# Kernel optimization log

Measured on AMD Instinct MI355X. Metric: run time of the kernel, lower is better.

Reference implementation:

```python
import jax, jax.numpy as jnp
import numpy as np

D_MODEL = 1024
NUM_HEADS = 16
D_K = D_MODEL // NUM_HEADS
B, N = 4, 2048


def setup_inputs() -> dict:
    key = jax.random.key(0)
    ks = jax.random.split(key, 5)
    scale = 1.0 / np.sqrt(D_MODEL)
    return {
        "x": jax.random.normal(ks[0], (B, N, D_MODEL), dtype=jnp.float32),
        "wq": jax.random.normal(ks[1], (D_MODEL, D_MODEL), dtype=jnp.float32) * scale,
        "wk": jax.random.normal(ks[2], (D_MODEL, D_MODEL), dtype=jnp.float32) * scale,
        "wv": jax.random.normal(ks[3], (D_MODEL, D_MODEL), dtype=jnp.float32) * scale,
        "wo": jax.random.normal(ks[4], (D_MODEL, D_MODEL), dtype=jnp.float32) * scale,
    }


def reference(x, wq, wk, wv, wo):
    b, n, d = x.shape
    # torch Linear(weight W) computes x @ W.T
    def proj(w):
        return (x @ w.T).reshape(b, n, NUM_HEADS, D_K).transpose(0, 2, 1, 3)  # [B,H,N,d_k]
    Q, K, V = proj(wq), proj(wk), proj(wv)
    scores = jnp.einsum("bhqd,bhkd->bhqk", Q, K) / jnp.sqrt(jnp.float32(D_K))
    causal = jnp.tril(jnp.ones((n, n), dtype=bool))
    scores = jnp.where(causal, scores, jnp.float32(-jnp.inf))
    attn = jax.nn.softmax(scores, axis=-1)
    vals = jnp.einsum("bhqk,bhkd->bhqd", attn, V)  # [B,H,N,d_k]
    vals = vals.transpose(0, 2, 1, 3).reshape(b, n, d)
    out = vals @ wo.T
    return (out, K, V)
```

## Files before the change

### kernel.cpp

```cpp
#include <hip/hip_runtime.h>
#include <hip/hip_bf16.h>

typedef __bf16 bf16_t;
typedef __bf16 bf16x8 __attribute__((ext_vector_type(8)));
typedef __bf16 bf16x4 __attribute__((ext_vector_type(4)));
typedef float f32x4 __attribute__((ext_vector_type(4)));
typedef float f32x16 __attribute__((ext_vector_type(16)));
typedef int i32x4 __attribute__((ext_vector_type(4)));

#define LDS_AS __attribute__((address_space(3)))
#define GLB_AS __attribute__((address_space(1)))

__device__ __forceinline__ void gload_lds16(const void* g, void* l) {
  __builtin_amdgcn_global_load_lds((const GLB_AS void*)g, (LDS_AS void*)l, 16, 0, 0);
}

static __device__ __forceinline__ f32x4 mfma16(bf16x8 a, bf16x8 b, f32x4 c) {
  return __builtin_amdgcn_mfma_f32_16x16x32_bf16(a, b, c, 0, 0, 0);
}
static __device__ __forceinline__ f32x16 mfma32(bf16x8 a, bf16x8 b, f32x16 c) {
  return __builtin_amdgcn_mfma_f32_32x32x16_bf16(a, b, c, 0, 0, 0);
}
__device__ __forceinline__ int cvtpk_bf16(float lo, float hi) {
  int r;
  asm("v_cvt_pk_bf16_f32 %0, %1, %2" : "=v"(r) : "v"(lo), "v"(hi));
  return r;
}
__device__ __forceinline__ bf16x8 mkfrag(int w0, int w1, int w2, int w3) {
  i32x4 v;
  v[0] = w0; v[1] = w1; v[2] = w2; v[3] = w3;
  return __builtin_bit_cast(bf16x8, v);
}

#define PIPE_TILE_END()                                        \
  asm volatile("s_waitcnt vmcnt(0)" ::: "memory");             \
  __builtin_amdgcn_s_barrier();                                \
  asm volatile("" ::: "memory");                               \
  __builtin_amdgcn_sched_barrier(0)

__device__ __forceinline__ void xcd_rc(int orig, int& rowI, int& colI) {
  int logical = ((orig & 7) << 6) | (orig >> 3);
  rowI = logical >> 3;
  colI = logical & 7;
}

#define QSCALE 0.18033688011112042f

__global__ __launch_bounds__(256) void cast_kernel(
    const float* __restrict__ x, const float* __restrict__ wq,
    const float* __restrict__ wk, const float* __restrict__ wv,
    const float* __restrict__ wo, bf16_t* __restrict__ xb,
    bf16_t* __restrict__ wqb, bf16_t* __restrict__ wkb,
    bf16_t* __restrict__ wvb, bf16_t* __restrict__ wob) {
  size_t i = ((size_t)blockIdx.x * 256 + threadIdx.x) * 4;
  const float* s;
  bf16_t* d;
  size_t off;
  if (i < 8388608) {
    s = x; d = xb; off = i;
  } else {
    size_t j = i - 8388608;
    int wi = (int)(j >> 20);
    off = j & 1048575;
    s = wi == 0 ? wq : wi == 1 ? wk : wi == 2 ? wv : wo;
    d = wi == 0 ? wqb : wi == 1 ? wkb : wi == 2 ? wvb : wob;
  }
  float4 v = *(const float4*)(s + off);
  bf16x4 o;
  o[0] = (bf16_t)v.x; o[1] = (bf16_t)v.y; o[2] = (bf16_t)v.z; o[3] = (bf16_t)v.w;
  *(bf16x4*)(d + off) = o;
}

__global__ __launch_bounds__(512) void gemm_qkv(
    const bf16_t* __restrict__ xb, const bf16_t* __restrict__ wqb,
    const bf16_t* __restrict__ wkb, const bf16_t* __restrict__ wvb,
    bf16_t* __restrict__ Qb, bf16_t* __restrict__ Kb, bf16_t* __restrict__ vTb,
    float* __restrict__ outK, float* __restrict__ outV) {
  __shared__ __align__(16) bf16_t lds[32768];
  const int tid = threadIdx.x;
  const int lane = tid & 63, w = tid >> 6;
  const int llo = lane & 15, lhi = lane >> 4;
  const int wm = w >> 2, wn = w & 3;
  int rowI, colI;
  xcd_rc(blockIdx.x, rowI, colI);
  const int rowBase = rowI * 128, colW = colI * 128;

  const int arow = tid >> 2, asrc = (tid & 3) ^ ((arow >> 1) & 3);
  const bf16_t* srcA = xb + (size_t)(rowBase + arow) * 1024 + asrc * 8;
  const bf16_t* srcB0 = wqb + (size_t)(colW + arow) * 1024 + asrc * 8;
  const bf16_t* srcB1 = wkb + (size_t)(colW + arow) * 1024 + asrc * 8;
  const bf16_t* srcB2 = wvb + (size_t)(colW + arow) * 1024 + asrc * 8;
  const int dstA = tid * 8;
  const int dstB0 = 4096 + tid * 8;
  const int dstB1 = 4096 + (512 + tid) * 8;
  const int dstB2 = 4096 + (1024 + tid) * 8;

  auto STAGE = [&](int kt, int b) {
    bf16_t* base = lds + b * 16384;
    gload_lds16(srcA + kt * 32, base + dstA);
    gload_lds16(srcB0 + kt * 32, base + dstB0);
    gload_lds16(srcB1 + kt * 32, base + dstB1);
    gload_lds16(srcB2 + kt * 32, base + dstB2);
  };

  f32x4 acc[4][6] = {};
  const int xr = (llo >> 1) & 3;
  STAGE(0, 0);
  PIPE_TILE_END();
  for (int kt = 0; kt < 32; ++kt) {
    if (kt + 1 < 32) STAGE(kt + 1, (kt + 1) & 1);
    __builtin_amdgcn_sched_barrier(0);
    const bf16_t* bufA = lds + (kt & 1) * 16384;
    const bf16_t* bufB = bufA + 4096;
    bf16x8 aF[4], bF[6];
#pragma unroll
    for (int mf = 0; mf < 4; ++mf)
      aF[mf] = *(const bf16x8*)&bufA[(wm * 64 + mf * 16 + llo) * 32 +
                                     ((lhi ^ xr) * 8)];
#pragma unroll
    for (int nf = 0; nf < 6; ++nf)
      bF[nf] = *(const bf16x8*)&bufB[(wn * 96 + nf * 16 + llo) * 32 +
                                     ((lhi ^ xr) * 8)];
    __builtin_amdgcn_s_setprio(1);
#pragma unroll
    for (int mf = 0; mf < 4; ++mf)
#pragma unroll
      for (int nf = 0; nf < 6; ++nf) acc[mf][nf] = mfma16(aF[mf], bF[nf], acc[mf][nf]);
    __builtin_amdgcn_s_setprio(0);
    PIPE_TILE_END();
  }

#pragma unroll
  for (int mf = 0; mf < 4; ++mf) {
    int m0 = rowBase + wm * 64 + mf * 16 + lhi * 4;
    int b = m0 >> 11, tok0 = m0 & 2047;
#pragma unroll
    for (int nf = 0; nf < 6; ++nf) {
      int n = wn * 96 + nf * 16 + llo;
      int mat = n >> 7;
      int nm = colW + (n & 127);
      int h = nm >> 6, dk = nm & 63;
      size_t hoff = ((size_t)(b * 16 + h) * 2048 + tok0) * 64 + dk;
      if (mat == 0) {
#pragma unroll
        for (int r = 0; r < 4; ++r)
          Qb[hoff + (size_t)r * 64] = (bf16_t)(acc[mf][nf][r] * QSCALE);
      } else if (mat == 1) {
#pragma unroll
        for (int r = 0; r < 4; ++r) {
          outK[hoff + (size_t)r * 64] = acc[mf][nf][r];
          Kb[hoff + (size_t)r * 64] = (bf16_t)acc[mf][nf][r];
        }
      } else {
#pragma unroll
        for (int r = 0; r < 4; ++r) outV[hoff + (size_t)r * 64] = acc[mf][nf][r];
        bf16x4 pk;
#pragma unroll
        for (int r = 0; r < 4; ++r) pk[r] = (bf16_t)acc[mf][nf][r];
        *(bf16x4*)&vTb[((size_t)(b * 16 + h) * 64 + dk) * 2048 + tok0] = pk;
      }
    }
  }
}

__global__ __launch_bounds__(256) void gemm_out(const bf16_t* __restrict__ valsb,
                                                const bf16_t* __restrict__ wob,
                                                float* __restrict__ out) {
  __shared__ __align__(16) bf16_t lds[16384];
  const int tid = threadIdx.x;
  const int lane = tid & 63, w = tid >> 6;
  const int llo = lane & 15, lhi = lane >> 4;
  const int wm = w >> 1, wn = w & 1;
  int rowI, colI;
  xcd_rc(blockIdx.x, rowI, colI);
  const int rowBase = rowI * 128, colW = colI * 128;

  int g0 = tid, g1 = 256 + tid;
  int r0 = g0 >> 2, r1 = g1 >> 2;
  int s0 = (g0 & 3) ^ ((r0 >> 1) & 3), s1 = (g1 & 3) ^ ((r1 >> 1) & 3);
  const bf16_t* srcA0 = valsb + (size_t)(rowBase + r0) * 1024 + s0 * 8;
  const bf16_t* srcA1 = valsb + (size_t)(rowBase + r1) * 1024 + s1 * 8;
  const bf16_t* srcB0 = wob + (size_t)(colW + r0) * 1024 + s0 * 8;
  const bf16_t* srcB1 = wob + (size_t)(colW + r1) * 1024 + s1 * 8;
  const int dA0 = g0 * 8, dA1 = g1 * 8;
  const int dB0 = 4096 + g0 * 8, dB1 = 4096 + g1 * 8;

  auto STAGE = [&](int kt, int b) {
    bf16_t* base = lds + b * 8192;
    gload_lds16(srcA0 + kt * 32, base + dA0);
    gload_lds16(srcA1 + kt * 32, base + dA1);
    gload_lds16(srcB0 + kt * 32, base + dB0);
    gload_lds16(srcB1 + kt * 32, base + dB1);
  };

  f32x4 acc[4][4] = {};
  const int xr = (llo >> 1) & 3;
  STAGE(0, 0);
  PIPE_TILE_END();
  for (int kt = 0; kt < 32; ++kt) {
    if (kt + 1 < 32) STAGE(kt + 1, (kt + 1) & 1);
    __builtin_amdgcn_sched_barrier(0);
    const bf16_t* bufA = lds + (kt & 1) * 8192;
    const bf16_t* bufB = bufA + 4096;
    bf16x8 aF[4], bF[4];
#pragma unroll
    for (int mf = 0; mf < 4; ++mf)
      aF[mf] = *(const bf16x8*)&bufA[(wm * 64 + mf * 16 + llo) * 32 +
                                     ((lhi ^ xr) * 8)];
#pragma unroll
    for (int nf = 0; nf < 4; ++nf)
      bF[nf] = *(const bf16x8*)&bufB[(wn * 64 + nf * 16 + llo) * 32 +
                                     ((lhi ^ xr) * 8)];
    __builtin_amdgcn_s_setprio(1);
#pragma unroll
    for (int mf = 0; mf < 4; ++mf)
#pragma unroll
      for (int nf = 0; nf < 4; ++nf) acc[mf][nf] = mfma16(aF[mf], bF[nf], acc[mf][nf]);
    __builtin_amdgcn_s_setprio(0);
    PIPE_TILE_END();
  }
#pragma unroll
  for (int mf = 0; mf < 4; ++mf) {
    int m0 = rowBase + wm * 64 + mf * 16 + lhi * 4;
#pragma unroll
    for (int nf = 0; nf < 4; ++nf) {
      int n = colW + wn * 64 + nf * 16 + llo;
#pragma unroll
      for (int r = 0; r < 4; ++r) out[(size_t)(m0 + r) * 1024 + n] = acc[mf][nf][r];
    }
  }
}

__global__ __launch_bounds__(256, 3) void attn_kernel(
    const bf16_t* __restrict__ Qb, const bf16_t* __restrict__ Kb,
    const bf16_t* __restrict__ vTb, bf16_t* __restrict__ valsb) {
  __shared__ bf16_t kS[2][64 * 64];
  __shared__ bf16_t vS[2][64 * 64];
  const int tid = threadIdx.x;
  const int w = tid >> 6, lane = tid & 63;
  const int ql = lane & 31, hi = lane >> 5, hi4 = hi * 4;
  const int head = blockIdx.x;
  const int qseg = 15 - blockIdx.y;
  const int qbase = qseg * 128;
  const int qw = qbase + w * 32;
  const int qrow = qw + ql;
  const int nkt = qseg * 2 + 2;
  const bf16_t* Qh = Qb + (size_t)head * 131072;
  const bf16_t* Kh = Kb + (size_t)head * 131072;
  const bf16_t* Vh = vTb + (size_t)head * 131072;

  bf16x8 qB[4];
#pragma unroll
  for (int kk = 0; kk < 4; ++kk)
    qB[kk] = *(const bf16x8*)&Qh[(size_t)qrow * 64 + kk * 16 + hi * 8];

  i32x4 ov;
  ov[0] = ov[1] = ov[2] = ov[3] = 0x3F803F80;
  const bf16x8 onesF = __builtin_bit_cast(bf16x8, ov);

  f32x16 oacc0 = {}, oacc1 = {};
  f32x16 lacc = {};

  const int c0 = tid, c1 = 256 + tid;
  const int r0 = c0 >> 3, r1 = c1 >> 3;
  const int s0 = (c0 & 7) ^ ((r0 ^ (r0 >> 3)) & 7);
  const int s1 = (c1 & 7) ^ ((r1 ^ (r1 >> 3)) & 7);

  auto STAGE = [&](int kt_, int bi) {
    const int kb_ = kt_ * 64;
    gload_lds16(Kh + (size_t)(kb_ + r0) * 64 + s0 * 8, &kS[bi][c0 * 8]);
    gload_lds16(Kh + (size_t)(kb_ + r1) * 64 + s1 * 8, &kS[bi][c1 * 8]);
    gload_lds16(Vh + (size_t)r0 * 2048 + kb_ + s0 * 8, &vS[bi][c0 * 8]);
    gload_lds16(Vh + (size_t)r1 * 2048 + kb_ + s1 * 8, &vS[bi][c1 * 8]);
  };

  const int swzA = (ql ^ (ql >> 3)) & 7;
  const int swzB = swzA ^ 4;

  STAGE(0, 0);
  __syncthreads();
  int cur = 0;
  for (int kt = 0; kt < nkt; ++kt) {
    const int kbase = kt * 64;
    if (kt + 1 < nkt) STAGE(kt + 1, cur ^ 1);
    if (kbase <= qw) {
      const bf16_t* kb = kS[cur];
      const bf16_t* vb = vS[cur];
      f32x16 st0 = {}, st1 = {};
      __builtin_amdgcn_s_setprio(1);
#pragma unroll
      for (int kk = 0; kk < 4; ++kk) {
        bf16x8 kf0 = *(const bf16x8*)&kb[ql * 64 + (((kk * 2 + hi) ^ swzA) * 8)];
        st0 = mfma32(kf0, qB[kk], st0);
      }
#pragma unroll
      for (int kk = 0; kk < 4; ++kk) {
        bf16x8 kf1 = *(const bf16x8*)&kb[(32 + ql) * 64 + (((kk * 2 + hi) ^ swzB) * 8)];
        st1 = mfma32(kf1, qB[kk], st1);
      }
      __builtin_amdgcn_s_setprio(0);
      if (kbase + 64 > qw) {
        const int lim = qrow - kbase;
#pragma unroll
        for (int rg = 0; rg < 16; ++rg) {
          const int kof = (rg & 3) + 8 * (rg >> 2) + hi4;
          if (kof > lim) st0[rg] = -__builtin_inff();
          if (kof + 32 > lim) st1[rg] = -__builtin_inff();
        }
      }
#pragma unroll
      for (int j = 0; j < 16; ++j) {
        st0[j] = __builtin_amdgcn_exp2f(st0[j]);
        st1[j] = __builtin_amdgcn_exp2f(st1[j]);
      }
      int a0 = cvtpk_bf16(st0[0], st0[1]), a1 = cvtpk_bf16(st0[2], st0[3]);
      int a2 = cvtpk_bf16(st0[4], st0[5]), a3 = cvtpk_bf16(st0[6], st0[7]);
      int a4 = cvtpk_bf16(st0[8], st0[9]), a5 = cvtpk_bf16(st0[10], st0[11]);
      int a6 = cvtpk_bf16(st0[12], st0[13]), a7 = cvtpk_bf16(st0[14], st0[15]);
      int b0 = cvtpk_bf16(st1[0], st1[1]), b1 = cvtpk_bf16(st1[2], st1[3]);
      int b2 = cvtpk_bf16(st1[4], st1[5]), b3 = cvtpk_bf16(st1[6], st1[7]);
      int b4 = cvtpk_bf16(st1[8], st1[9]), b5 = cvtpk_bf16(st1[10], st1[11]);
      int b6 = cvtpk_bf16(st1[12], st1[13]), b7 = cvtpk_bf16(st1[14], st1[15]);
      auto s02 = __builtin_amdgcn_permlane32_swap(a0, a2, false, false);
      auto s13 = __builtin_amdgcn_permlane32_swap(a1, a3, false, false);
      auto s46 = __builtin_amdgcn_permlane32_swap(a4, a6, false, false);
      auto s57 = __builtin_amdgcn_permlane32_swap(a5, a7, false, false);
      auto t02 = __builtin_amdgcn_permlane32_swap(b0, b2, false, false);
      auto t13 = __builtin_amdgcn_permlane32_swap(b1, b3, false, false);
      auto t46 = __builtin_amdgcn_permlane32_swap(b4, b6, false, false);
      auto t57 = __builtin_amdgcn_permlane32_swap(b5, b7, false, false);
      bf16x8 pB0 = mkfrag(s02[0], s13[0], s02[1], s13[1]);
      bf16x8 pB1 = mkfrag(s46[0], s57[0], s46[1], s57[1]);
      bf16x8 pB2 = mkfrag(t02[0], t13[0], t02[1], t13[1]);
      bf16x8 pB3 = mkfrag(t46[0], t57[0], t46[1], t57[1]);
      __builtin_amdgcn_s_setprio(1);
#pragma unroll
      for (int ks = 0; ks < 4; ++ks) {
        bf16x8 pb = ks == 0 ? pB0 : ks == 1 ? pB1 : ks == 2 ? pB2 : pB3;
        bf16x8 vf0 = *(const bf16x8*)&vb[ql * 64 + (((ks * 2 + hi) ^ swzA) * 8)];
        oacc0 = mfma32(vf0, pb, oacc0);
        bf16x8 vf1 = *(const bf16x8*)&vb[(32 + ql) * 64 + (((ks * 2 + hi) ^ swzB) * 8)];
        oacc1 = mfma32(vf1, pb, oacc1);
        lacc = mfma32(onesF, pb, lacc);
      }
      __builtin_amdgcn_s_setprio(0);
    }
    __syncthreads();
    cur ^= 1;
  }
  const float inv = 1.f / lacc[0];
  size_t base = ((size_t)(head >> 4) * 2048 + qrow) * 1024 + (head & 15) * 64 + hi4;
#pragma unroll
  for (int rg = 0; rg < 4; ++rg) {
    bf16x4 o0, o1;
#pragma unroll
    for (int j = 0; j < 4; ++j) {
      o0[j] = (bf16_t)(oacc0[rg * 4 + j] * inv);
      o1[j] = (bf16_t)(oacc1[rg * 4 + j] * inv);
    }
    *(bf16x4*)&valsb[base + rg * 8] = o0;
    *(bf16x4*)&valsb[base + 32 + rg * 8] = o1;
  }
}

extern "C" void kernel_launch(void* const* d_in, const int* in_sizes, int n_in,
                              void* d_out, int out_size, void* d_ws, size_t ws_size,
                              hipStream_t stream) {
  const float* x = (const float*)d_in[0];
  const float* wq = (const float*)d_in[1];
  const float* wk = (const float*)d_in[2];
  const float* wv = (const float*)d_in[3];
  const float* wo = (const float*)d_in[4];
  float* out = (float*)d_out;
  float* outK = out + 8388608;
  float* outV = out + 16777216;
  bf16_t* xb = (bf16_t*)d_ws;
  bf16_t* wqb = xb + 8388608;
  bf16_t* wkb = wqb + 1048576;
  bf16_t* wvb = wkb + 1048576;
  bf16_t* wob = wvb + 1048576;
  bf16_t* Qb = wob + 1048576;
  bf16_t* Kb = Qb + 8388608;
  bf16_t* vTb = Kb + 8388608;
  bf16_t* valsb = vTb + 8388608;
  cast_kernel<<<12288, 256, 0, stream>>>(x, wq, wk, wv, wo, xb, wqb, wkb, wvb, wob);
  gemm_qkv<<<512, 512, 0, stream>>>(xb, wqb, wkb, wvb, Qb, Kb, vTb, outK, outV);
  attn_kernel<<<dim3(64, 16), 256, 0, stream>>>(Qb, Kb, vTb, valsb);
  gemm_out<<<512, 256, 0, stream>>>(valsb, wob, out);
}
```

Measured before the change: 160.3 us.

## Split attention key range across two wave groups and reduce partials in LDS

The attention block grows from 256 to 512 threads, and two groups of four waves each process alternating 64-key tiles of a 128-key stage. At the end, the partial output accumulators and row sums are combined through LDS. The row sum is now computed from the exponentials with VALU adds plus a lane shuffle, replacing the extra ones-matrix MFMA per step. This aims to double the waves working on each query tile and drop one MFMA per k-step, at the cost of an LDS reduction, a final sync, and launch bounds that allow one block per CU.

```diff
diff --git a/kernel.cpp b/kernel.cpp
--- a/kernel.cpp
+++ b/kernel.cpp
@@ -166,7 +166,7 @@
 __global__ __launch_bounds__(256) void gemm_out(const bf16_t* __restrict__ valsb,
                                                 const bf16_t* __restrict__ wob,
                                                 float* __restrict__ out) {
-  __shared__ __align__(16) bf16_t lds[16384];
+  __shared__ __align__(16) bf16_t slds[16384];
   const int tid = threadIdx.x;
   const int lane = tid & 63, w = tid >> 6;
   const int llo = lane & 15, lhi = lane >> 4;
@@ -186,7 +186,7 @@
   const int dB0 = 4096 + g0 * 8, dB1 = 4096 + g1 * 8;
 
   auto STAGE = [&](int kt, int b) {
-    bf16_t* base = lds + b * 8192;
+    bf16_t* base = slds + b * 8192;
     gload_lds16(srcA0 + kt * 32, base + dA0);
     gload_lds16(srcA1 + kt * 32, base + dA1);
     gload_lds16(srcB0 + kt * 32, base + dB0);
@@ -200,7 +200,7 @@
   for (int kt = 0; kt < 32; ++kt) {
     if (kt + 1 < 32) STAGE(kt + 1, (kt + 1) & 1);
     __builtin_amdgcn_sched_barrier(0);
-    const bf16_t* bufA = lds + (kt & 1) * 8192;
+    const bf16_t* bufA = slds + (kt & 1) * 8192;
     const bf16_t* bufB = bufA + 4096;
     bf16x8 aF[4], bF[4];
 #pragma unroll
@@ -231,20 +231,21 @@
   }
 }
 
-__global__ __launch_bounds__(256, 3) void attn_kernel(
+__global__ __launch_bounds__(512, 1) void attn_kernel(
     const bf16_t* __restrict__ Qb, const bf16_t* __restrict__ Kb,
     const bf16_t* __restrict__ vTb, bf16_t* __restrict__ valsb) {
-  __shared__ bf16_t kS[2][64 * 64];
-  __shared__ bf16_t vS[2][64 * 64];
+  __shared__ bf16_t kS[2][2][4096];
+  __shared__ bf16_t vS[2][2][4096];
   const int tid = threadIdx.x;
   const int w = tid >> 6, lane = tid & 63;
+  const int g = w >> 2, wq = w & 3;
   const int ql = lane & 31, hi = lane >> 5, hi4 = hi * 4;
   const int head = blockIdx.x;
   const int qseg = 15 - blockIdx.y;
   const int qbase = qseg * 128;
-  const int qw = qbase + w * 32;
+  const int qw = qbase + wq * 32;
   const int qrow = qw + ql;
-  const int nkt = qseg * 2 + 2;
+  const int nsi = qseg + 1;
   const bf16_t* Qh = Qb + (size_t)head * 131072;
   const bf16_t* Kh = Kb + (size_t)head * 131072;
   const bf16_t* Vh = vTb + (size_t)head * 131072;
@@ -254,38 +255,33 @@
   for (int kk = 0; kk < 4; ++kk)
     qB[kk] = *(const bf16x8*)&Qh[(size_t)qrow * 64 + kk * 16 + hi * 8];
 
-  i32x4 ov;
-  ov[0] = ov[1] = ov[2] = ov[3] = 0x3F803F80;
-  const bf16x8 onesF = __builtin_bit_cast(bf16x8, ov);
-
   f32x16 oacc0 = {}, oacc1 = {};
-  f32x16 lacc = {};
-
-  const int c0 = tid, c1 = 256 + tid;
-  const int r0 = c0 >> 3, r1 = c1 >> 3;
-  const int s0 = (c0 & 7) ^ ((r0 ^ (r0 >> 3)) & 7);
-  const int s1 = (c1 & 7) ^ ((r1 ^ (r1 >> 3)) & 7);
-
-  auto STAGE = [&](int kt_, int bi) {
-    const int kb_ = kt_ * 64;
-    gload_lds16(Kh + (size_t)(kb_ + r0) * 64 + s0 * 8, &kS[bi][c0 * 8]);
-    gload_lds16(Kh + (size_t)(kb_ + r1) * 64 + s1 * 8, &kS[bi][c1 * 8]);
-    gload_lds16(Vh + (size_t)r0 * 2048 + kb_ + s0 * 8, &vS[bi][c0 * 8]);
-    gload_lds16(Vh + (size_t)r1 * 2048 + kb_ + s1 * 8, &vS[bi][c1 * 8]);
+  float lsum = 0.f;
+
+  const int sr = tid >> 3;
+  const int sc = (tid & 7) ^ ((sr ^ (sr >> 3)) & 7);
+
+  auto STAGE = [&](int si) {
+    const int p = si & 1;
+    const int ka = si * 128;
+    const int kb2 = ka + 64;
+    gload_lds16(Kh + (size_t)(ka + sr) * 64 + sc * 8, &kS[p][0][tid * 8]);
+    gload_lds16(Vh + (size_t)sr * 2048 + ka + sc * 8, &vS[p][0][tid * 8]);
+    gload_lds16(Kh + (size_t)(kb2 + sr) * 64 + sc * 8, &kS[p][1][tid * 8]);
+    gload_lds16(Vh + (size_t)sr * 2048 + kb2 + sc * 8, &vS[p][1][tid * 8]);
   };
 
   const int swzA = (ql ^ (ql >> 3)) & 7;
   const int swzB = swzA ^ 4;
 
-  STAGE(0, 0);
+  STAGE(0);
   __syncthreads();
-  int cur = 0;
-  for (int kt = 0; kt < nkt; ++kt) {
-    const int kbase = kt * 64;
-    if (kt + 1 < nkt) STAGE(kt + 1, cur ^ 1);
+  for (int si = 0; si < nsi; ++si) {
+    if (si + 1 < nsi) STAGE(si + 1);
+    const int kbase = si * 128 + g * 64;
     if (kbase <= qw) {
-      const bf16_t* kb = kS[cur];
-      const bf16_t* vb = vS[cur];
+      const bf16_t* kb = kS[si & 1][g];
+      const bf16_t* vb = vS[si & 1][g];
       f32x16 st0 = {}, st1 = {};
       __builtin_amdgcn_s_setprio(1);
 #pragma unroll
@@ -308,11 +304,21 @@
           if (kof + 32 > lim) st1[rg] = -__builtin_inff();
         }
       }
-#pragma unroll
-      for (int j = 0; j < 16; ++j) {
-        st0[j] = __builtin_amdgcn_exp2f(st0[j]);
-        st1[j] = __builtin_amdgcn_exp2f(st1[j]);
-      }
+      float r0 = 0.f, r1 = 0.f, r2 = 0.f, r3 = 0.f;
+#pragma unroll
+      for (int rg = 0; rg < 16; rg += 4) {
+        st0[rg] = __builtin_amdgcn_exp2f(st0[rg]);         r0 += st0[rg];
+        st0[rg + 1] = __builtin_amdgcn_exp2f(st0[rg + 1]); r1 += st0[rg + 1];
+        st0[rg + 2] = __builtin_amdgcn_exp2f(st0[rg + 2]); r2 += st0[rg + 2];
+        st0[rg + 3] = __builtin_amdgcn_exp2f(st0[rg + 3]); r3 += st0[rg + 3];
+        st1[rg] = __builtin_amdgcn_exp2f(st1[rg]);         r0 += st1[rg];
+        st1[rg + 1] = __builtin_amdgcn_exp2f(st1[rg + 1]); r1 += st1[rg + 1];
+        st1[rg + 2] = __builtin_amdgcn_exp2f(st1[rg + 2]); r2 += st1[rg + 2];
+        st1[rg + 3] = __builtin_amdgcn_exp2f(st1[rg + 3]); r3 += st1[rg + 3];
+      }
+      float rs = (r0 + r1) + (r2 + r3);
+      rs += __shfl_xor(rs, 32);
+      lsum += rs;
       int a0 = cvtpk_bf16(st0[0], st0[1]), a1 = cvtpk_bf16(st0[2], st0[3]);
       int a2 = cvtpk_bf16(st0[4], st0[5]), a3 = cvtpk_bf16(st0[6], st0[7]);
       int a4 = cvtpk_bf16(st0[8], st0[9]), a5 = cvtpk_bf16(st0[10], st0[11]);
@@ -341,25 +347,44 @@
         oacc0 = mfma32(vf0, pb, oacc0);
         bf16x8 vf1 = *(const bf16x8*)&vb[(32 + ql) * 64 + (((ks * 2 + hi) ^ swzB) * 8)];
         oacc1 = mfma32(vf1, pb, oacc1);
-        lacc = mfma32(onesF, pb, lacc);
       }
       __builtin_amdgcn_s_setprio(0);
     }
     __syncthreads();
-    cur ^= 1;
-  }
-  const float inv = 1.f / lacc[0];
-  size_t base = ((size_t)(head >> 4) * 2048 + qrow) * 1024 + (head & 15) * 64 + hi4;
-#pragma unroll
-  for (int rg = 0; rg < 4; ++rg) {
-    bf16x4 o0, o1;
-#pragma unroll
-    for (int j = 0; j < 4; ++j) {
-      o0[j] = (bf16_t)(oacc0[rg * 4 + j] * inv);
-      o1[j] = (bf16_t)(oacc1[rg * 4 + j] * inv);
-    }
-    *(bf16x4*)&valsb[base + rg * 8] = o0;
-    *(bf16x4*)&valsb[base + 32 + rg * 8] = o1;
+  }
+
+  float* oBuf = (float*)&kS[0][0][0];
+  float* lBuf = (float*)&vS[0][0][0];
+  const int t = wq * 64 + lane;
+  if (g == 1) {
+#pragma unroll
+    for (int j = 0; j < 16; ++j) {
+      oBuf[j * 256 + t] = oacc0[j];
+      oBuf[(16 + j) * 256 + t] = oacc1[j];
+    }
+    lBuf[t] = lsum;
+  }
+  __syncthreads();
+  if (g == 0) {
+#pragma unroll
+    for (int j = 0; j < 16; ++j) {
+      oacc0[j] += oBuf[j * 256 + t];
+      oacc1[j] += oBuf[(16 + j) * 256 + t];
+    }
+    lsum += lBuf[t];
+    const float inv = 1.f / lsum;
+    size_t base = ((size_t)(head >> 4) * 2048 + qrow) * 1024 + (head & 15) * 64 + hi4;
+#pragma unroll
+    for (int rg = 0; rg < 4; ++rg) {
+      bf16x4 o0, o1;
+#pragma unroll
+      for (int j = 0; j < 4; ++j) {
+        o0[j] = (bf16_t)(oacc0[rg * 4 + j] * inv);
+        o1[j] = (bf16_t)(oacc1[rg * 4 + j] * inv);
+      }
+      *(bf16x4*)&valsb[base + rg * 8] = o0;
+      *(bf16x4*)&valsb[base + 32 + rg * 8] = o1;
+    }
   }
 }
 
@@ -385,6 +410,6 @@
   bf16_t* valsb = vTb + 8388608;
   cast_kernel<<<12288, 256, 0, stream>>>(x, wq, wk, wv, wo, xb, wqb, wkb, wvb, wob);
   gemm_qkv<<<512, 512, 0, stream>>>(xb, wqb, wkb, wvb, Qb, Kb, vTb, outK, outV);
-  attn_kernel<<<dim3(64, 16), 256, 0, stream>>>(Qb, Kb, vTb, valsb);
+  attn_kernel<<<dim3(64, 16), 512, 0, stream>>>(Qb, Kb, vTb, valsb);
   gemm_out<<<512, 256, 0, stream>>>(valsb, wob, out);
 }
```

After: 162.3 us. No clear change (+1.3%).
